# Kernel optimization log

Hardware: AMD Instinct MI355X
Metric: run time of the kernel (lower is better)

## Reference

```python
import jax, jax.numpy as jnp
import numpy as np

B, L, D, H = 2, 2048, 1024, 16
DH = D // H
NEG = -10000.0

def setup_inputs() -> dict:
    key = jax.random.key(0)
    ks = jax.random.split(key, 6)
    scale = 1.0 / np.sqrt(D)
    inp = {
        "x": jax.random.normal(ks[0], (B, L, D), dtype=jnp.float32),
        "m": jnp.ones((B, L), dtype=jnp.int32),  # 1 = valid token, 0 = padded
        "Wq": jax.random.normal(ks[1], (D, D), dtype=jnp.float32) * scale,
        "bq": jnp.zeros((D,), dtype=jnp.float32),
        "Wk": jax.random.normal(ks[2], (D, D), dtype=jnp.float32) * scale,
        "bk": jnp.zeros((D,), dtype=jnp.float32),
        "Wv": jax.random.normal(ks[3], (D, D), dtype=jnp.float32) * scale,
        "bv": jnp.zeros((D,), dtype=jnp.float32),
        "Wp": jax.random.normal(ks[4], (D, D), dtype=jnp.float32) * scale,
        "bp": jnp.zeros((D,), dtype=jnp.float32),
    }
    return inp

def reference(x, m, Wq, bq, Wk, bk, Wv, bv, Wp, bp):
    # torch Linear: x @ W.T + b
    def heads(t):  # (B,L,D) -> (B,H,L,DH)
        return t.reshape(B, L, H, DH).transpose(0, 2, 1, 3)
    q = heads(x @ Wq.T + bq)
    k = heads(x @ Wk.T + bk)
    v = heads(x @ Wv.T + bv)
    att = jnp.einsum("bhqd,bhkd->bhqk", q, k) * (1.0 / np.sqrt(DH))  # (B,H,L,L)
    causal = jnp.tril(jnp.ones((L, L), dtype=bool))[None, None]       # (1,1,L,L)
    att = jnp.where(causal, att, NEG)
    # additive key-padding mask: 0 for valid, -10000 for padded keys
    pad = (1.0 - m.astype(att.dtype))[:, None, None, :] * NEG         # (B,1,1,L)
    att = att + pad
    att = jax.nn.softmax(att, axis=-1)
    y = jnp.einsum("bhqk,bhkd->bhqd", att, v)                          # (B,H,L,DH)
    y = y.transpose(0, 2, 1, 3).reshape(B, L, D)
    return y @ Wp.T + bp
```

## Files before the change

kernel.cpp:

```cpp
#include <hip/hip_runtime.h>
#include <hip/hip_bf16.h>

#define NB 2
#define NL 2048
#define ND 1024
#define NH 16
#define NDH 64
#define NM (NB*NL)

typedef unsigned short u16;
typedef __attribute__((ext_vector_type(8))) short short8;
typedef __attribute__((ext_vector_type(4))) float floatx4;

__device__ __forceinline__ u16 f2bf(float f) {
  union { float f; unsigned int u; } v; v.f = f;
  unsigned int r = v.u + 0x7FFF + ((v.u >> 16) & 1);
  return (u16)(r >> 16);
}

__device__ __forceinline__ void async_cp16(u16* lds, const u16* g) {
  __builtin_amdgcn_global_load_lds(
      (const __attribute__((address_space(1))) void*)g,
      (__attribute__((address_space(3))) void*)lds, 16, 0, 0);
}

__global__ __launch_bounds__(256)
void cvt_all(const float* __restrict__ wq, const float* __restrict__ wk,
             const float* __restrict__ wv, const float* __restrict__ wp,
             const float* __restrict__ x,
             u16* __restrict__ ow, u16* __restrict__ ox)
{
  const int per4 = ND * ND / 4;
  const int tot  = 4 * per4 + NM * ND / 4;
  for (int t = blockIdx.x * 256 + threadIdx.x; t < tot; t += gridDim.x * 256) {
    const float* src; uint2* dst; int off;
    if (t < 4 * per4) {
      int w = t >> 18; off = t & (per4 - 1);
      src = (w == 0) ? wq : (w == 1) ? wk : (w == 2) ? wv : wp;
      dst = (uint2*)(ow + (size_t)w * ND * ND);
    } else {
      off = t - 4 * per4; src = x; dst = (uint2*)ox;
    }
    float4 f = ((const float4*)src)[off];
    u16 h[4] = { f2bf(f.x), f2bf(f.y), f2bf(f.z), f2bf(f.w) };
    dst[off] = *(const uint2*)h;
  }
}

#define BM 128
#define BN 128
#define BK 32
#define LDT 32

template<bool C_F32>
__global__ __launch_bounds__(256)
void gemm_bt_bias(const u16* __restrict__ A,
                  const u16* __restrict__ W0, const u16* __restrict__ W1, const u16* __restrict__ W2,
                  const float* __restrict__ B0, const float* __restrict__ B1, const float* __restrict__ B2,
                  void* __restrict__ C0, void* __restrict__ C1, void* __restrict__ C2,
                  float scale0)
{
  const int z = blockIdx.z;
  const u16* W    = (z == 0) ? W0 : (z == 1) ? W1 : W2;
  const float* Bi = (z == 0) ? B0 : (z == 1) ? B1 : B2;
  void* C         = (z == 0) ? C0 : (z == 1) ? C1 : C2;
  const float sc  = (z == 0) ? scale0 : 1.0f;

  const int n0 = blockIdx.x * BN;
  const int m0 = blockIdx.y * BM;
  const int tid  = threadIdx.x;
  const int lane = tid & 63;
  const int wave = tid >> 6;
  const int wm = (wave >> 1) * 64;
  const int wn = (wave & 1) * 64;
  const int quad = lane >> 4;
  const int l16  = lane & 15;

  __shared__ u16 As[BM * LDT];
  __shared__ u16 Bs[BN * LDT];

  floatx4 acc[4][4];
#pragma unroll
  for (int i = 0; i < 4; ++i)
#pragma unroll
    for (int j = 0; j < 4; ++j)
      acc[i][j] = (floatx4){0.f, 0.f, 0.f, 0.f};

  for (int k0 = 0; k0 < ND; k0 += BK) {
#pragma unroll
    for (int it = 0; it < 2; ++it) {
      int idx = tid + it * 256;
      int rr  = idx >> 2;
      int c8  = (idx & 3) << 3;
      async_cp16(&Bs[idx * 8], &W[(size_t)(n0 + rr) * ND + k0 + c8]);
      async_cp16(&As[idx * 8], &A[(size_t)(m0 + rr) * ND + k0 + c8]);
    }
    __syncthreads();

    short8 af[4], bfr[4];
#pragma unroll
    for (int i = 0; i < 4; ++i)
      af[i] = *(const short8*)&As[(wm + i * 16 + l16) * LDT + quad * 8];
#pragma unroll
    for (int j = 0; j < 4; ++j)
      bfr[j] = *(const short8*)&Bs[(wn + j * 16 + l16) * LDT + quad * 8];

#pragma unroll
    for (int i = 0; i < 4; ++i)
#pragma unroll
      for (int j = 0; j < 4; ++j)
        acc[i][j] = __builtin_amdgcn_mfma_f32_16x16x32_bf16(af[i], bfr[j], acc[i][j], 0, 0, 0);
    __syncthreads();
  }

#pragma unroll
  for (int j = 0; j < 4; ++j) {
    const int ncol = n0 + wn + j * 16 + l16;
    const float bv = Bi[ncol];
#pragma unroll
    for (int i = 0; i < 4; ++i) {
      const int mbase = m0 + wm + i * 16 + quad * 4;
#pragma unroll
      for (int r2 = 0; r2 < 4; ++r2) {
        float v = (acc[i][j][r2] + bv) * sc;
        if (C_F32) ((float*)C)[(size_t)(mbase + r2) * ND + ncol] = v;
        else       ((u16*)C)[(size_t)(mbase + r2) * ND + ncol] = f2bf(v);
      }
    }
  }
}

#define KC 64
#define PSTR 72

__global__ __launch_bounds__(256)
void attn_mfma(const u16* __restrict__ Q, const u16* __restrict__ K,
               const u16* __restrict__ V, const int* __restrict__ msk,
               u16* __restrict__ Y)
{
  const int qt = gridDim.x - 1 - blockIdx.x;
  const int bh = blockIdx.y;
  const int b = bh >> 4;
  const int h = bh & 15;
  const int q0 = qt * 64;
  const int tid  = threadIdx.x;
  const int lane = tid & 63;
  const int wave = tid >> 6;
  const int wq   = wave * 16;
  const int quad = lane >> 4;
  const int l16  = lane & 15;

  __shared__ u16 Ks[KC][PSTR];
  __shared__ u16 Vt[NDH][PSTR];
  __shared__ u16 Ps[64][PSTR];
  __shared__ u16 Ms[NL];

  for (int j = tid; j < NL; j += 256) Ms[j] = (u16)(msk[b * NL + j] ? 1 : 0);

  short8 qf[2];
#pragma unroll
  for (int kk = 0; kk < 2; ++kk)
    qf[kk] = *(const short8*)&Q[(size_t)(b * NL + q0 + wq + l16) * ND
                                + h * NDH + kk * 32 + quad * 8];

  short8 onesf;
  {
    const short ov = (l16 == 0) ? (short)0x3F80 : (short)0;
#pragma unroll
    for (int e = 0; e < 8; ++e) onesf[e] = ov;
  }

  floatx4 o[4];
#pragma unroll
  for (int ot = 0; ot < 4; ++ot) o[ot] = (floatx4){0.f, 0.f, 0.f, 0.f};
  floatx4 lacc = (floatx4){0.f, 0.f, 0.f, 0.f};

  const int nchunks = qt + 1;
  for (int kc = 0; kc < nchunks; ++kc) {
    const int k0 = kc * KC;

#pragma unroll
    for (int p = 0; p < 2; ++p) {
      int idx = tid + p * 256;
      int r = idx >> 3, c = (idx & 7) << 3;
      *(uint4*)&Ks[r][c] = *(const uint4*)&K[(size_t)(b * NL + k0 + r) * ND + h * NDH + c];
    }
    {
      int rv = (tid & 31) * 2;
      int c  = (tid >> 5) * 8;
      uint4 va = *(const uint4*)&V[(size_t)(b * NL + k0 + rv)     * ND + h * NDH + c];
      uint4 vb = *(const uint4*)&V[(size_t)(b * NL + k0 + rv + 1) * ND + h * NDH + c];
      const u16* ap = (const u16*)&va;
      const u16* bp = (const u16*)&vb;
#pragma unroll
      for (int e = 0; e < 8; ++e)
        *(unsigned int*)&Vt[c + e][rv] = (unsigned int)ap[e] | ((unsigned int)bp[e] << 16);
    }
    __syncthreads();

    floatx4 s[4];
#pragma unroll
    for (int ct = 0; ct < 4; ++ct) {
      short8 kf0 = *(const short8*)&Ks[ct * 16 + l16][quad * 8];
      short8 kf1 = *(const short8*)&Ks[ct * 16 + l16][32 + quad * 8];
      floatx4 a = (floatx4){0.f, 0.f, 0.f, 0.f};
      a = __builtin_amdgcn_mfma_f32_16x16x32_bf16(qf[0], kf0, a, 0, 0, 0);
      a = __builtin_amdgcn_mfma_f32_16x16x32_bf16(qf[1], kf1, a, 0, 0, 0);
      s[ct] = a;
    }

    float pmul[4]; int col[4];
#pragma unroll
    for (int ct = 0; ct < 4; ++ct) {
      col[ct]  = k0 + ct * 16 + l16;
      pmul[ct] = (float)Ms[col[ct]];
    }
    const bool diag = (kc == qt);
#pragma unroll
    for (int ct = 0; ct < 4; ++ct)
#pragma unroll
      for (int r2 = 0; r2 < 4; ++r2) {
        float p = pmul[ct] * __expf(s[ct][r2]);
        if (diag) {
          const int row = q0 + wq + quad * 4 + r2;
          p = (col[ct] > row) ? 0.f : p;
        }
        Ps[wq + quad * 4 + r2][ct * 16 + l16] = f2bf(p);
      }

#pragma unroll
    for (int kk = 0; kk < 2; ++kk) {
      short8 pf = *(const short8*)&Ps[wq + l16][kk * 32 + quad * 8];
#pragma unroll
      for (int ot = 0; ot < 4; ++ot) {
        short8 vf = *(const short8*)&Vt[ot * 16 + l16][kk * 32 + quad * 8];
        o[ot] = __builtin_amdgcn_mfma_f32_16x16x32_bf16(pf, vf, o[ot], 0, 0, 0);
      }
      lacc = __builtin_amdgcn_mfma_f32_16x16x32_bf16(pf, onesf, lacc, 0, 0, 0);
    }
    __syncthreads();
  }

  float inv[4];
#pragma unroll
  for (int r2 = 0; r2 < 4; ++r2) {
    const float l = __shfl(lacc[r2], quad << 4);
    inv[r2] = 1.0f / l;
  }
#pragma unroll
  for (int ot = 0; ot < 4; ++ot)
#pragma unroll
    for (int r2 = 0; r2 < 4; ++r2) {
      const int row = q0 + wq + quad * 4 + r2;
      Y[(size_t)(b * NL + row) * ND + h * NDH + ot * 16 + l16] = f2bf(o[ot][r2] * inv[r2]);
    }
}

extern "C" void kernel_launch(void* const* d_in, const int* in_sizes, int n_in,
                              void* d_out, int out_size, void* d_ws, size_t ws_size,
                              hipStream_t stream) {
  const float* x  = (const float*)d_in[0];
  const int*   m  = (const int*)d_in[1];
  const float* Wq = (const float*)d_in[2];
  const float* bq = (const float*)d_in[3];
  const float* Wk = (const float*)d_in[4];
  const float* bk = (const float*)d_in[5];
  const float* Wv = (const float*)d_in[6];
  const float* bv = (const float*)d_in[7];
  const float* Wp = (const float*)d_in[8];
  const float* bp = (const float*)d_in[9];
  float* out = (float*)d_out;

  const size_t per = (size_t)NM * ND;
  u16* Qb = (u16*)d_ws;
  u16* Kb = Qb + per;
  u16* Vb = Kb + per;
  u16* Wb = Vb + per;
  u16* Yb = Qb;
  u16* xb = (u16*)d_out;

  cvt_all<<<2048, 256, 0, stream>>>(Wq, Wk, Wv, Wp, x, Wb, xb);

  dim3 gq(ND / BN, NM / BM, 3);
  gemm_bt_bias<false><<<gq, 256, 0, stream>>>(
      xb, Wb, Wb + (size_t)ND * ND, Wb + 2 * (size_t)ND * ND,
      bq, bk, bv, (void*)Qb, (void*)Kb, (void*)Vb, 0.125f);

  attn_mfma<<<dim3(NL / 64, NB * NH), 256, 0, stream>>>(Qb, Kb, Vb, m, Yb);

  dim3 gp(ND / BN, NM / BM, 1);
  const u16* Wpb = Wb + 3 * (size_t)ND * ND;
  gemm_bt_bias<true><<<gp, 256, 0, stream>>>(
      Yb, Wpb, Wpb, Wpb, bp, bp, bp,
      (void*)out, (void*)out, (void*)out, 1.0f);
}
```

Before: 227.0 us.

## Double query tile per attention block and pack P stores via DPP

Each attention workgroup now handles 128 query rows (32 per wave) instead of 64, so every K/V chunk loaded into LDS feeds twice as many MFMAs and global K/V traffic per query is halved. Probability writes to LDS are packed into 32-bit stores by exchanging neighbour values with a DPP lane swap, and the mask preload is trimmed to the causal range. The grid shrinks to half as many blocks, which lowers parallelism and raises register pressure per wave. Causal masking now applies to the last two chunks.

```diff
diff --git a/kernel.cpp b/kernel.cpp
--- a/kernel.cpp
+++ b/kernel.cpp
@@ -22,6 +22,10 @@
   __builtin_amdgcn_global_load_lds(
       (const __attribute__((address_space(1))) void*)g,
       (__attribute__((address_space(3))) void*)lds, 16, 0, 0);
+}
+
+__device__ __forceinline__ unsigned dpp_xor1(unsigned v) {
+  return (unsigned)__builtin_amdgcn_mov_dpp((int)v, 0xB1, 0xF, 0xF, true);
 }
 
 __global__ __launch_bounds__(256)
@@ -142,26 +146,30 @@
   const int bh = blockIdx.y;
   const int b = bh >> 4;
   const int h = bh & 15;
-  const int q0 = qt * 64;
+  const int q0 = qt * 128;
   const int tid  = threadIdx.x;
   const int lane = tid & 63;
   const int wave = tid >> 6;
-  const int wq   = wave * 16;
+  const int wq   = wave * 32;
   const int quad = lane >> 4;
   const int l16  = lane & 15;
 
   __shared__ u16 Ks[KC][PSTR];
   __shared__ u16 Vt[NDH][PSTR];
-  __shared__ u16 Ps[64][PSTR];
+  __shared__ u16 Ps[128][PSTR];
   __shared__ u16 Ms[NL];
 
-  for (int j = tid; j < NL; j += 256) Ms[j] = (u16)(msk[b * NL + j] ? 1 : 0);
-
-  short8 qf[2];
-#pragma unroll
-  for (int kk = 0; kk < 2; ++kk)
-    qf[kk] = *(const short8*)&Q[(size_t)(b * NL + q0 + wq + l16) * ND
-                                + h * NDH + kk * 32 + quad * 8];
+  const int nchunks = 2 * qt + 2;
+
+  for (int j = tid; j < nchunks * KC; j += 256) Ms[j] = (u16)(msk[b * NL + j] ? 1 : 0);
+
+  short8 qf[2][2];
+#pragma unroll
+  for (int rb = 0; rb < 2; ++rb)
+#pragma unroll
+    for (int kk = 0; kk < 2; ++kk)
+      qf[rb][kk] = *(const short8*)&Q[(size_t)(b * NL + q0 + wq + rb * 16 + l16) * ND
+                                      + h * NDH + kk * 32 + quad * 8];
 
   short8 onesf;
   {
@@ -170,12 +178,15 @@
     for (int e = 0; e < 8; ++e) onesf[e] = ov;
   }
 
-  floatx4 o[4];
-#pragma unroll
-  for (int ot = 0; ot < 4; ++ot) o[ot] = (floatx4){0.f, 0.f, 0.f, 0.f};
-  floatx4 lacc = (floatx4){0.f, 0.f, 0.f, 0.f};
-
-  const int nchunks = qt + 1;
+  floatx4 o[2][4];
+#pragma unroll
+  for (int rb = 0; rb < 2; ++rb)
+#pragma unroll
+    for (int ot = 0; ot < 4; ++ot) o[rb][ot] = (floatx4){0.f, 0.f, 0.f, 0.f};
+  floatx4 lacc[2];
+  lacc[0] = (floatx4){0.f, 0.f, 0.f, 0.f};
+  lacc[1] = (floatx4){0.f, 0.f, 0.f, 0.f};
+
   for (int kc = 0; kc < nchunks; ++kc) {
     const int k0 = kc * KC;
 
@@ -198,15 +209,18 @@
     }
     __syncthreads();
 
-    floatx4 s[4];
+    floatx4 s[2][4];
 #pragma unroll
     for (int ct = 0; ct < 4; ++ct) {
       short8 kf0 = *(const short8*)&Ks[ct * 16 + l16][quad * 8];
       short8 kf1 = *(const short8*)&Ks[ct * 16 + l16][32 + quad * 8];
-      floatx4 a = (floatx4){0.f, 0.f, 0.f, 0.f};
-      a = __builtin_amdgcn_mfma_f32_16x16x32_bf16(qf[0], kf0, a, 0, 0, 0);
-      a = __builtin_amdgcn_mfma_f32_16x16x32_bf16(qf[1], kf1, a, 0, 0, 0);
-      s[ct] = a;
+#pragma unroll
+      for (int rb = 0; rb < 2; ++rb) {
+        floatx4 a = (floatx4){0.f, 0.f, 0.f, 0.f};
+        a = __builtin_amdgcn_mfma_f32_16x16x32_bf16(qf[rb][0], kf0, a, 0, 0, 0);
+        a = __builtin_amdgcn_mfma_f32_16x16x32_bf16(qf[rb][1], kf1, a, 0, 0, 0);
+        s[rb][ct] = a;
+      }
     }
 
     float pmul[4]; int col[4];
@@ -215,45 +229,67 @@
       col[ct]  = k0 + ct * 16 + l16;
       pmul[ct] = (float)Ms[col[ct]];
     }
-    const bool diag = (kc == qt);
-#pragma unroll
-    for (int ct = 0; ct < 4; ++ct)
-#pragma unroll
-      for (int r2 = 0; r2 < 4; ++r2) {
-        float p = pmul[ct] * __expf(s[ct][r2]);
-        if (diag) {
-          const int row = q0 + wq + quad * 4 + r2;
-          p = (col[ct] > row) ? 0.f : p;
+    const bool causal = (kc >= 2 * qt);
+    const int odd  = l16 & 1;
+#pragma unroll
+    for (int rb = 0; rb < 2; ++rb) {
+      const int rowb = q0 + wq + rb * 16 + quad * 4;
+#pragma unroll
+      for (int ct = 0; ct < 4; ++ct) {
+        unsigned bb[4];
+#pragma unroll
+        for (int r2 = 0; r2 < 4; ++r2) {
+          float p = pmul[ct] * __expf(s[rb][ct][r2]);
+          if (causal) p = (col[ct] > rowb + r2) ? 0.f : p;
+          bb[r2] = (unsigned)f2bf(p);
         }
-        Ps[wq + quad * 4 + r2][ct * 16 + l16] = f2bf(p);
-      }
+        unsigned n0v = dpp_xor1(bb[0]), n1v = dpp_xor1(bb[1]);
+        unsigned n2v = dpp_xor1(bb[2]), n3v = dpp_xor1(bb[3]);
+        const int colb = ct * 16 + (l16 & ~1);
+        const int row01 = wq + rb * 16 + quad * 4 + odd;
+        unsigned d01 = odd ? (n1v | (bb[1] << 16)) : (bb[0] | (n0v << 16));
+        unsigned d23 = odd ? (n3v | (bb[3] << 16)) : (bb[2] | (n2v << 16));
+        *(unsigned*)&Ps[row01][colb]     = d01;
+        *(unsigned*)&Ps[row01 + 2][colb] = d23;
+      }
+    }
 
 #pragma unroll
     for (int kk = 0; kk < 2; ++kk) {
-      short8 pf = *(const short8*)&Ps[wq + l16][kk * 32 + quad * 8];
+      short8 pf[2];
+#pragma unroll
+      for (int rb = 0; rb < 2; ++rb)
+        pf[rb] = *(const short8*)&Ps[wq + rb * 16 + l16][kk * 32 + quad * 8];
 #pragma unroll
       for (int ot = 0; ot < 4; ++ot) {
         short8 vf = *(const short8*)&Vt[ot * 16 + l16][kk * 32 + quad * 8];
-        o[ot] = __builtin_amdgcn_mfma_f32_16x16x32_bf16(pf, vf, o[ot], 0, 0, 0);
-      }
-      lacc = __builtin_amdgcn_mfma_f32_16x16x32_bf16(pf, onesf, lacc, 0, 0, 0);
+#pragma unroll
+        for (int rb = 0; rb < 2; ++rb)
+          o[rb][ot] = __builtin_amdgcn_mfma_f32_16x16x32_bf16(pf[rb], vf, o[rb][ot], 0, 0, 0);
+      }
+      lacc[0] = __builtin_amdgcn_mfma_f32_16x16x32_bf16(pf[0], onesf, lacc[0], 0, 0, 0);
+      lacc[1] = __builtin_amdgcn_mfma_f32_16x16x32_bf16(pf[1], onesf, lacc[1], 0, 0, 0);
     }
     __syncthreads();
   }
 
-  float inv[4];
-#pragma unroll
-  for (int r2 = 0; r2 < 4; ++r2) {
-    const float l = __shfl(lacc[r2], quad << 4);
-    inv[r2] = 1.0f / l;
-  }
-#pragma unroll
-  for (int ot = 0; ot < 4; ++ot)
+#pragma unroll
+  for (int rb = 0; rb < 2; ++rb) {
+    float inv[4];
 #pragma unroll
     for (int r2 = 0; r2 < 4; ++r2) {
-      const int row = q0 + wq + quad * 4 + r2;
-      Y[(size_t)(b * NL + row) * ND + h * NDH + ot * 16 + l16] = f2bf(o[ot][r2] * inv[r2]);
-    }
+      const float l = __shfl(lacc[rb][r2], quad << 4);
+      inv[r2] = 1.0f / l;
+    }
+#pragma unroll
+    for (int ot = 0; ot < 4; ++ot)
+#pragma unroll
+      for (int r2 = 0; r2 < 4; ++r2) {
+        const int row = q0 + wq + rb * 16 + quad * 4 + r2;
+        Y[(size_t)(b * NL + row) * ND + h * NDH + ot * 16 + l16] =
+            f2bf(o[rb][ot][r2] * inv[r2]);
+      }
+  }
 }
 
 extern "C" void kernel_launch(void* const* d_in, const int* in_sizes, int n_in,
@@ -286,7 +322,7 @@
       xb, Wb, Wb + (size_t)ND * ND, Wb + 2 * (size_t)ND * ND,
       bq, bk, bv, (void*)Qb, (void*)Kb, (void*)Vb, 0.125f);
 
-  attn_mfma<<<dim3(NL / 64, NB * NH), 256, 0, stream>>>(Qb, Kb, Vb, m, Yb);
+  attn_mfma<<<dim3(NL / 128, NB * NH), 256, 0, stream>>>(Qb, Kb, Vb, m, Yb);
 
   dim3 gp(ND / BN, NM / BM, 1);
   const u16* Wpb = Wb + 3 * (size_t)ND * ND;
```

Result: slower. 246.7 us (+8.7%).

## Pre-transpose V in a separate kernel and read K/V fragments directly from global

Applied to the files above, without the earlier changes.

Adds a vtrans kernel that writes V per head in transposed layout. The attention kernel then loads K and V^T MFMA fragments straight from global memory instead of staging them through LDS, which removes the per-chunk block barriers and the LDS mask table. P is written to LDS as packed 32-bit pairs using a DPP lane swap, so there are half as many LDS stores. The cost is an extra kernel launch and extra global traffic, with every wave loading K/V separately and relying on cache hits. VT is placed in the output buffer after the converted x.

```diff
diff --git a/kernel.cpp b/kernel.cpp
--- a/kernel.cpp
+++ b/kernel.cpp
@@ -22,6 +22,10 @@
   __builtin_amdgcn_global_load_lds(
       (const __attribute__((address_space(1))) void*)g,
       (__attribute__((address_space(3))) void*)lds, 16, 0, 0);
+}
+
+__device__ __forceinline__ unsigned dpp_xor1(unsigned v) {
+  return (unsigned)__builtin_amdgcn_mov_dpp((int)v, 0xB1, 0xF, 0xF, true);
 }
 
 __global__ __launch_bounds__(256)
@@ -130,12 +134,40 @@
   }
 }
 
+#define TSTR 66
+__global__ __launch_bounds__(256)
+void vtrans(const u16* __restrict__ V, u16* __restrict__ VT)
+{
+  const int lt = blockIdx.x;
+  const int bh = blockIdx.y;
+  const int b = bh >> 4, h = bh & 15;
+  const int l0 = lt * 64;
+  const int tid = threadIdx.x;
+  __shared__ u16 Ls[64][TSTR];
+#pragma unroll
+  for (int p = 0; p < 2; ++p) {
+    int idx = tid + p * 256;
+    int r = idx >> 3, c = (idx & 7) << 3;
+    *(uint4*)&Ls[r][c] = *(const uint4*)&V[(size_t)(b * NL + l0 + r) * ND + h * NDH + c];
+  }
+  __syncthreads();
+#pragma unroll
+  for (int p = 0; p < 2; ++p) {
+    int idx = tid + p * 256;
+    int lg = idx & 7, d = idx >> 3;
+    u16 tb[8];
+#pragma unroll
+    for (int e = 0; e < 8; ++e) tb[e] = Ls[lg * 8 + e][d];
+    *(uint4*)&VT[((size_t)(b * NH + h) * NDH + d) * NL + l0 + lg * 8] = *(const uint4*)tb;
+  }
+}
+
 #define KC 64
 #define PSTR 72
 
 __global__ __launch_bounds__(256)
 void attn_mfma(const u16* __restrict__ Q, const u16* __restrict__ K,
-               const u16* __restrict__ V, const int* __restrict__ msk,
+               const u16* __restrict__ VT, const int* __restrict__ msk,
                u16* __restrict__ Y)
 {
   const int qt = gridDim.x - 1 - blockIdx.x;
@@ -150,12 +182,11 @@
   const int quad = lane >> 4;
   const int l16  = lane & 15;
 
-  __shared__ u16 Ks[KC][PSTR];
-  __shared__ u16 Vt[NDH][PSTR];
   __shared__ u16 Ps[64][PSTR];
-  __shared__ u16 Ms[NL];
-
-  for (int j = tid; j < NL; j += 256) Ms[j] = (u16)(msk[b * NL + j] ? 1 : 0);
+
+  const u16* Kbase  = K  + (size_t)b * NL * ND + h * NDH;
+  const u16* VTbase = VT + (size_t)(b * NH + h) * NDH * NL;
+  const int* mbase  = msk + b * NL;
 
   short8 qf[2];
 #pragma unroll
@@ -175,70 +206,56 @@
   for (int ot = 0; ot < 4; ++ot) o[ot] = (floatx4){0.f, 0.f, 0.f, 0.f};
   floatx4 lacc = (floatx4){0.f, 0.f, 0.f, 0.f};
 
-  const int nchunks = qt + 1;
-  for (int kc = 0; kc < nchunks; ++kc) {
+  const int odd = l16 & 1;
+  for (int kc = 0; kc <= qt; ++kc) {
     const int k0 = kc * KC;
 
-#pragma unroll
-    for (int p = 0; p < 2; ++p) {
-      int idx = tid + p * 256;
-      int r = idx >> 3, c = (idx & 7) << 3;
-      *(uint4*)&Ks[r][c] = *(const uint4*)&K[(size_t)(b * NL + k0 + r) * ND + h * NDH + c];
-    }
-    {
-      int rv = (tid & 31) * 2;
-      int c  = (tid >> 5) * 8;
-      uint4 va = *(const uint4*)&V[(size_t)(b * NL + k0 + rv)     * ND + h * NDH + c];
-      uint4 vb = *(const uint4*)&V[(size_t)(b * NL + k0 + rv + 1) * ND + h * NDH + c];
-      const u16* ap = (const u16*)&va;
-      const u16* bp = (const u16*)&vb;
-#pragma unroll
-      for (int e = 0; e < 8; ++e)
-        *(unsigned int*)&Vt[c + e][rv] = (unsigned int)ap[e] | ((unsigned int)bp[e] << 16);
-    }
-    __syncthreads();
-
     floatx4 s[4];
 #pragma unroll
     for (int ct = 0; ct < 4; ++ct) {
-      short8 kf0 = *(const short8*)&Ks[ct * 16 + l16][quad * 8];
-      short8 kf1 = *(const short8*)&Ks[ct * 16 + l16][32 + quad * 8];
+      const u16* kr = Kbase + (size_t)(k0 + ct * 16 + l16) * ND;
+      short8 kf0 = *(const short8*)(kr + quad * 8);
+      short8 kf1 = *(const short8*)(kr + 32 + quad * 8);
       floatx4 a = (floatx4){0.f, 0.f, 0.f, 0.f};
       a = __builtin_amdgcn_mfma_f32_16x16x32_bf16(qf[0], kf0, a, 0, 0, 0);
       a = __builtin_amdgcn_mfma_f32_16x16x32_bf16(qf[1], kf1, a, 0, 0, 0);
       s[ct] = a;
     }
 
-    float pmul[4]; int col[4];
+    const bool diag = (kc == qt);
+    const int rowb = q0 + wq + quad * 4;
 #pragma unroll
     for (int ct = 0; ct < 4; ++ct) {
-      col[ct]  = k0 + ct * 16 + l16;
-      pmul[ct] = (float)Ms[col[ct]];
-    }
-    const bool diag = (kc == qt);
-#pragma unroll
-    for (int ct = 0; ct < 4; ++ct)
+      const int col = k0 + ct * 16 + l16;
+      const float pmul = (float)mbase[col];
+      unsigned bb[4];
 #pragma unroll
       for (int r2 = 0; r2 < 4; ++r2) {
-        float p = pmul[ct] * __expf(s[ct][r2]);
-        if (diag) {
-          const int row = q0 + wq + quad * 4 + r2;
-          p = (col[ct] > row) ? 0.f : p;
-        }
-        Ps[wq + quad * 4 + r2][ct * 16 + l16] = f2bf(p);
+        float p = pmul * __expf(s[ct][r2]);
+        if (diag) p = (col > rowb + r2) ? 0.f : p;
+        bb[r2] = (unsigned)f2bf(p);
       }
+      unsigned n0v = dpp_xor1(bb[0]), n1v = dpp_xor1(bb[1]);
+      unsigned n2v = dpp_xor1(bb[2]), n3v = dpp_xor1(bb[3]);
+      const int colb  = ct * 16 + (l16 & ~1);
+      const int row01 = wq + quad * 4 + odd;
+      unsigned d01 = odd ? (n1v | (bb[1] << 16)) : (bb[0] | (n0v << 16));
+      unsigned d23 = odd ? (n3v | (bb[3] << 16)) : (bb[2] | (n2v << 16));
+      *(unsigned*)&Ps[row01][colb]     = d01;
+      *(unsigned*)&Ps[row01 + 2][colb] = d23;
+    }
 
 #pragma unroll
     for (int kk = 0; kk < 2; ++kk) {
       short8 pf = *(const short8*)&Ps[wq + l16][kk * 32 + quad * 8];
 #pragma unroll
       for (int ot = 0; ot < 4; ++ot) {
-        short8 vf = *(const short8*)&Vt[ot * 16 + l16][kk * 32 + quad * 8];
+        short8 vf = *(const short8*)(VTbase + (size_t)(ot * 16 + l16) * NL
+                                     + k0 + kk * 32 + quad * 8);
         o[ot] = __builtin_amdgcn_mfma_f32_16x16x32_bf16(pf, vf, o[ot], 0, 0, 0);
       }
       lacc = __builtin_amdgcn_mfma_f32_16x16x32_bf16(pf, onesf, lacc, 0, 0, 0);
     }
-    __syncthreads();
   }
 
   float inv[4];
@@ -278,6 +295,7 @@
   u16* Wb = Vb + per;
   u16* Yb = Qb;
   u16* xb = (u16*)d_out;
+  u16* VTb = xb + per;
 
   cvt_all<<<2048, 256, 0, stream>>>(Wq, Wk, Wv, Wp, x, Wb, xb);
 
@@ -286,7 +304,9 @@
       xb, Wb, Wb + (size_t)ND * ND, Wb + 2 * (size_t)ND * ND,
       bq, bk, bv, (void*)Qb, (void*)Kb, (void*)Vb, 0.125f);
 
-  attn_mfma<<<dim3(NL / 64, NB * NH), 256, 0, stream>>>(Qb, Kb, Vb, m, Yb);
+  vtrans<<<dim3(NL / 64, NB * NH), 256, 0, stream>>>(Vb, VTb);
+
+  attn_mfma<<<dim3(NL / 64, NB * NH), 256, 0, stream>>>(Qb, Kb, VTb, m, Yb);
 
   dim3 gp(ND / BN, NM / BM, 1);
   const u16* Wpb = Wb + 3 * (size_t)ND * ND;
```

After: 383.5 us. +68.9%, slower.

## Reorder attention block schedule and pack P stores via DPP lane exchange

Applied to the files above, without the earlier changes.

The attention grid becomes a 1D launch of 1024 blocks. Blocks are mapped to query tiles in a zig-zag order of long, long, short, short, so heavy causal tiles are interleaved with light ones across (batch, head) groups. The P tile write now pairs neighbouring lanes with a DPP xor-1 swap, so each lane stores 32-bit packed pairs instead of 16-bit scalars, halving LDS store instructions. The mask preload now only covers the key range the block actually visits, at the cost of a more complex index mapping.

```diff
diff --git a/kernel.cpp b/kernel.cpp
--- a/kernel.cpp
+++ b/kernel.cpp
@@ -22,6 +22,10 @@
   __builtin_amdgcn_global_load_lds(
       (const __attribute__((address_space(1))) void*)g,
       (__attribute__((address_space(3))) void*)lds, 16, 0, 0);
+}
+
+__device__ __forceinline__ unsigned dpp_xor1(unsigned v) {
+  return (unsigned)__builtin_amdgcn_mov_dpp((int)v, 0xB1, 0xF, 0xF, true);
 }
 
 __global__ __launch_bounds__(256)
@@ -138,8 +142,11 @@
                const u16* __restrict__ V, const int* __restrict__ msk,
                u16* __restrict__ Y)
 {
-  const int qt = gridDim.x - 1 - blockIdx.x;
-  const int bh = blockIdx.y;
+  const int t = blockIdx.x;
+  const int r = t >> 8;
+  const int s = t & 7;
+  const int bh = (t & 255) >> 3;
+  const int qt = (r == 0) ? 31 - s : (r == 1) ? 16 + s : (r == 2) ? 15 - s : s;
   const int b = bh >> 4;
   const int h = bh & 15;
   const int q0 = qt * 64;
@@ -155,7 +162,9 @@
   __shared__ u16 Ps[64][PSTR];
   __shared__ u16 Ms[NL];
 
-  for (int j = tid; j < NL; j += 256) Ms[j] = (u16)(msk[b * NL + j] ? 1 : 0);
+  const int nchunks = qt + 1;
+
+  for (int j = tid; j < nchunks * KC; j += 256) Ms[j] = (u16)(msk[b * NL + j] ? 1 : 0);
 
   short8 qf[2];
 #pragma unroll
@@ -175,15 +184,15 @@
   for (int ot = 0; ot < 4; ++ot) o[ot] = (floatx4){0.f, 0.f, 0.f, 0.f};
   floatx4 lacc = (floatx4){0.f, 0.f, 0.f, 0.f};
 
-  const int nchunks = qt + 1;
+  const int odd = l16 & 1;
   for (int kc = 0; kc < nchunks; ++kc) {
     const int k0 = kc * KC;
 
 #pragma unroll
     for (int p = 0; p < 2; ++p) {
       int idx = tid + p * 256;
-      int r = idx >> 3, c = (idx & 7) << 3;
-      *(uint4*)&Ks[r][c] = *(const uint4*)&K[(size_t)(b * NL + k0 + r) * ND + h * NDH + c];
+      int rr = idx >> 3, c = (idx & 7) << 3;
+      *(uint4*)&Ks[rr][c] = *(const uint4*)&K[(size_t)(b * NL + k0 + rr) * ND + h * NDH + c];
     }
     {
       int rv = (tid & 31) * 2;
@@ -198,7 +207,7 @@
     }
     __syncthreads();
 
-    floatx4 s[4];
+    floatx4 sc[4];
 #pragma unroll
     for (int ct = 0; ct < 4; ++ct) {
       short8 kf0 = *(const short8*)&Ks[ct * 16 + l16][quad * 8];
@@ -206,27 +215,31 @@
       floatx4 a = (floatx4){0.f, 0.f, 0.f, 0.f};
       a = __builtin_amdgcn_mfma_f32_16x16x32_bf16(qf[0], kf0, a, 0, 0, 0);
       a = __builtin_amdgcn_mfma_f32_16x16x32_bf16(qf[1], kf1, a, 0, 0, 0);
-      s[ct] = a;
-    }
-
-    float pmul[4]; int col[4];
+      sc[ct] = a;
+    }
+
+    const bool diag = (kc == qt);
+    const int rowb = q0 + wq + quad * 4;
 #pragma unroll
     for (int ct = 0; ct < 4; ++ct) {
-      col[ct]  = k0 + ct * 16 + l16;
-      pmul[ct] = (float)Ms[col[ct]];
-    }
-    const bool diag = (kc == qt);
-#pragma unroll
-    for (int ct = 0; ct < 4; ++ct)
+      const int col = k0 + ct * 16 + l16;
+      const float pmul = (float)Ms[col];
+      unsigned bb[4];
 #pragma unroll
       for (int r2 = 0; r2 < 4; ++r2) {
-        float p = pmul[ct] * __expf(s[ct][r2]);
-        if (diag) {
-          const int row = q0 + wq + quad * 4 + r2;
-          p = (col[ct] > row) ? 0.f : p;
-        }
-        Ps[wq + quad * 4 + r2][ct * 16 + l16] = f2bf(p);
+        float p = pmul * __expf(sc[ct][r2]);
+        if (diag) p = (col > rowb + r2) ? 0.f : p;
+        bb[r2] = (unsigned)f2bf(p);
       }
+      unsigned n0v = dpp_xor1(bb[0]), n1v = dpp_xor1(bb[1]);
+      unsigned n2v = dpp_xor1(bb[2]), n3v = dpp_xor1(bb[3]);
+      const int colb  = ct * 16 + (l16 & ~1);
+      const int row01 = wq + quad * 4 + odd;
+      unsigned d01 = odd ? (n1v | (bb[1] << 16)) : (bb[0] | (n0v << 16));
+      unsigned d23 = odd ? (n3v | (bb[3] << 16)) : (bb[2] | (n2v << 16));
+      *(unsigned*)&Ps[row01][colb]     = d01;
+      *(unsigned*)&Ps[row01 + 2][colb] = d23;
+    }
 
 #pragma unroll
     for (int kk = 0; kk < 2; ++kk) {
@@ -286,7 +299,7 @@
       xb, Wb, Wb + (size_t)ND * ND, Wb + 2 * (size_t)ND * ND,
       bq, bk, bv, (void*)Qb, (void*)Kb, (void*)Vb, 0.125f);
 
-  attn_mfma<<<dim3(NL / 64, NB * NH), 256, 0, stream>>>(Qb, Kb, Vb, m, Yb);
+  attn_mfma<<<1024, 256, 0, stream>>>(Qb, Kb, Vb, m, Yb);
 
   dim3 gp(ND / BN, NM / BM, 1);
   const u16* Wpb = Wb + 3 * (size_t)ND * ND;
```

Result: faster. 215.7 us (-5.0%).
